# Kernel tuning notes

Hardware: AMD Instinct MI355X
Metric: run time of the kernel (lower is better)

The kernel has to match this reference:

```python
import jax, jax.numpy as jnp
import numpy as np

N_ATOMS = 8000
N_PAIRS = 80000
NF_IN = 32
NF_OUT = 32
N_DIST = 16
N_COMP = 4      # l_max=1: [l=0 (1), l=1 (3)] tensor components
N_INV = 2       # _invariant_counts[(2, 1)]
MIND_SOFT = 0.85
MAXD_SOFT = 5.0
HARD_CUTOFF = 6.5
GN_EPS = 1e-5


def _sensitivity(dist, mu, sigma):
    # HIP-NN style inverse-distance Gaussians with smooth cos^2 cutoff.
    inv_d = 1.0 / dist                                   # (P,)
    base = jnp.exp(-0.5 * ((inv_d[:, None] - mu) / sigma) ** 2)  # (P, n_dist)
    cut = jnp.where(dist < HARD_CUTOFF,
                    jnp.cos(0.5 * jnp.pi * dist / HARD_CUTOFF) ** 2, 0.0)
    return base * cut[:, None]


def setup_inputs() -> dict:
    key = jax.random.key(0)
    ks = jax.random.split(key, 10)
    in_features = jax.random.normal(ks[0], (N_ATOMS, NF_IN), jnp.float32)
    pair_first = jnp.sort(jax.random.randint(ks[1], (N_PAIRS,), 0, N_ATOMS))
    pair_second = jax.random.randint(ks[2], (N_PAIRS,), 0, N_ATOMS)
    dist_pairs = (0.5 + (HARD_CUTOFF - 0.5)
                  * jax.random.uniform(ks[3], (N_PAIRS,), jnp.float32))
    tensor_rhats = jax.random.normal(ks[4], (N_PAIRS, N_COMP), jnp.float32)
    # learned params
    sens_mu = jnp.linspace(1.0 / MAXD_SOFT, 1.0 / MIND_SOFT, N_DIST).astype(jnp.float32)
    sens_sigma = jnp.full((N_DIST,), float(sens_mu[1] - sens_mu[0]), jnp.float32)
    s_int = (2.0 / (N_DIST * NF_IN + NF_OUT)) ** 0.5
    int_weights = s_int * jax.random.normal(ks[5], (N_DIST, NF_OUT, NF_IN), jnp.float32)
    s_self = (2.0 / (NF_IN + NF_OUT)) ** 0.5
    selfint_w = s_self * jax.random.normal(ks[6], (NF_OUT, NF_IN), jnp.float32)
    selfint_b = jnp.zeros((NF_OUT,), jnp.float32)
    s_mix = (2.0 / (N_INV * NF_OUT + NF_OUT)) ** 0.5
    mixing_weights = s_mix * jax.random.normal(ks[7], (NF_OUT, N_INV, NF_OUT), jnp.float32)
    gn_weight = jnp.ones((N_INV * NF_OUT,), jnp.float32)
    gn_bias = jnp.zeros((N_INV * NF_OUT,), jnp.float32)
    return {
        "in_features": in_features, "tensor_rhats": tensor_rhats,
        "dist_pairs": dist_pairs, "int_weights": int_weights,
        "selfint_w": selfint_w, "selfint_b": selfint_b,
        "mixing_weights": mixing_weights, "gn_weight": gn_weight,
        "gn_bias": gn_bias, "sens_mu": sens_mu, "sens_sigma": sens_sigma,
        "pair_first": pair_first, "pair_second": pair_second,
    }


def reference(in_features, tensor_rhats, dist_pairs, int_weights,
              selfint_w, selfint_b, mixing_weights, gn_weight, gn_bias,
              sens_mu, sens_sigma, pair_first, pair_second):
    n_atoms = in_features.shape[0]
    # self interaction (Linear)
    self_part = in_features @ selfint_w.T + selfint_b          # (N, nf_out)
    # tensor sensitivities: (P, n_comp, n_dist) -> flat (P, n_comp*n_dist)
    sense = _sensitivity(dist_pairs, sens_mu, sens_sigma)      # (P, n_dist)
    sense_flat = (tensor_rhats[:, :, None] * sense[:, None, :]).reshape(
        -1, N_COMP * N_DIST)
    # envsum: env[a, s, f] = sum_{p: pair_first[p]=a} sense_flat[p, s] * feat[pair_second[p], f]
    feat_j = in_features[pair_second]                          # (P, nf_in)
    contrib = sense_flat[:, :, None] * feat_j[:, None, :]      # (P, S, nf_in)
    env = jax.ops.segment_sum(contrib, pair_first, num_segments=n_atoms)
    # interaction weights contraction
    w_rs = jnp.transpose(int_weights, (0, 2, 1)).reshape(N_DIST * NF_IN, NF_OUT)
    env_rs = env.reshape(n_atoms * N_COMP, N_DIST * NF_IN)
    tf = (env_rs @ w_rs).reshape(n_atoms, N_COMP, NF_OUT)
    tf = jnp.transpose(tf, (0, 2, 1))                          # (N, nf_out, n_comp)
    # HopInvariantLayer (n_max=2, l_max=1): [l=0 scalar, |l=1 vector|^2]
    invariants = jnp.stack(
        [tf[..., 0], jnp.sum(tf[..., 1:] ** 2, axis=-1)], axis=-1)  # (N, nf_out, 2)
    # GroupNorm over channels (n_inv groups of nf_out channels)
    x = jnp.transpose(invariants, (0, 2, 1))                   # (N, n_inv, nf_out)
    mean = jnp.mean(x, axis=-1, keepdims=True)
    var = jnp.var(x, axis=-1, keepdims=True)
    xn = (x - mean) / jnp.sqrt(var + GN_EPS)
    xn = xn * gn_weight.reshape(N_INV, NF_OUT) + gn_bias.reshape(N_INV, NF_OUT)
    norm_inv = jnp.transpose(xn, (0, 2, 1)).reshape(n_atoms, NF_OUT * N_INV)
    mix = norm_inv @ mixing_weights.reshape(NF_OUT * N_INV, NF_OUT)
    return mix + self_part
```

## Files before the change

### kernel.cpp

```cpp
#include <hip/hip_runtime.h>
#include <hip/hip_bf16.h>
#include <stdint.h>

#define GN_EPS 1e-5f

typedef __fp16 half2_t __attribute__((ext_vector_type(2)));
typedef __fp16 v8h __attribute__((ext_vector_type(8)));
typedef float v4f __attribute__((ext_vector_type(4)));
union U32H2 { uint32_t u; half2_t h; };
union U4V8 { uint4 u; v8h h; };
union UF { uint32_t u; float f; };

__device__ __forceinline__ float ldin(const void* p, int i, bool bf) {
    if (bf) {
        UF c; c.u = ((uint32_t)((const uint16_t*)p)[i]) << 16;
        return c.f;
    }
    return ((const float*)p)[i];
}

__device__ __forceinline__ uint16_t f2bf(float x) {
    union { float f; uint32_t u; } c; c.f = x;
    uint32_t u = c.u;
    return (uint16_t)((u + 0x7FFFu + ((u >> 16) & 1u)) >> 16);
}

__device__ __forceinline__ bool detect_bf16(const void* gnw) {
    uint32_t det = *(const uint32_t*)gnw;
    return (det >> 16) == (det & 0xFFFFu);
}

__device__ __forceinline__ uint32_t pkh2(float lo, float hi) {
    U32H2 u; u.h = __builtin_amdgcn_cvt_pkrtz(lo, hi); return u.u;
}

__global__ __launch_bounds__(256) void k0_prep(
    const void* __restrict__ feat, const void* __restrict__ rhats,
    const void* __restrict__ dists, const void* __restrict__ intw,
    const void* __restrict__ selfw, const void* __restrict__ selfb,
    const void* __restrict__ mw, const void* __restrict__ gnw,
    const void* __restrict__ gnb, const void* __restrict__ mu,
    const void* __restrict__ sig, const int* __restrict__ pf,
    int* __restrict__ seg, uint32_t* __restrict__ Wmf,
    float* __restrict__ featf, float4* __restrict__ rc4,
    float2* __restrict__ dj2, const int* __restrict__ ps,
    float* __restrict__ mwf, uint32_t* __restrict__ selfh,
    float* __restrict__ gnwf, float* __restrict__ gnbf,
    float* __restrict__ selfbf, float* __restrict__ muf,
    float* __restrict__ isgf, int n_atoms, int n_pairs)
{
    const bool bf = detect_bf16(gnw);
    const int tid = blockIdx.x * 256 + threadIdx.x;

    if (tid < n_pairs) {
        int a0 = pf[tid];
        if (tid == 0) { for (int a = 0; a <= a0; ++a) seg[a] = 0; }
        if (tid + 1 < n_pairs) {
            int a1 = pf[tid + 1];
            for (int a = a0 + 1; a <= a1; ++a) seg[a] = tid + 1;
        } else {
            for (int a = a0 + 1; a <= n_atoms; ++a) seg[a] = n_pairs;
        }
        float dist = ldin(dists, tid, bf);
        float cd = __cosf(0.2416609733530613f * dist);
        float cut = (dist < 6.5f) ? cd * cd : 0.0f;
        float4 rc;
        rc.x = ldin(rhats, 4 * tid + 0, bf) * cut;
        rc.y = ldin(rhats, 4 * tid + 1, bf) * cut;
        rc.z = ldin(rhats, 4 * tid + 2, bf) * cut;
        rc.w = ldin(rhats, 4 * tid + 3, bf) * cut;
        rc4[tid] = rc;
        float2 dj; dj.x = 1.0f / dist; dj.y = __int_as_float(ps[tid]);
        dj2[tid] = dj;
    }
    {
        int i0 = tid * 4;
#pragma unroll
        for (int k = 0; k < 4; ++k) {
            int i = i0 + k;
            if (i < n_atoms * 32) featf[i] = ldin(feat, i, bf);
        }
    }
    if (tid < 8192) {
        int fp = tid & 15, d = (tid >> 4) & 15, o = tid >> 8;
        float wlo = ldin(intw, (d * 32 + o) * 32 + 2 * fp, bf);
        float whi = ldin(intw, (d * 32 + o) * 32 + 2 * fp + 1, bf);
        Wmf[tid] = pkh2(wlo, whi);
    }
    if (tid < 2048) mwf[tid] = ldin(mw, tid, bf);
    if (tid < 512) {
        int fp = tid & 15, o = tid >> 4;
        selfh[tid] = pkh2(ldin(selfw, o * 32 + 2 * fp, bf),
                          ldin(selfw, o * 32 + 2 * fp + 1, bf));
    }
    if (tid < 64) { gnwf[tid] = ldin(gnw, tid, bf); gnbf[tid] = ldin(gnb, tid, bf); }
    if (tid < 32) selfbf[tid] = ldin(selfb, tid, bf);
    if (tid < 16) { muf[tid] = ldin(mu, tid, bf); isgf[tid] = 1.0f / ldin(sig, tid, bf); }
}

__global__ __launch_bounds__(256, 4) void k2_main(
    const int* __restrict__ seg, const uint32_t* __restrict__ Wmf,
    const float* __restrict__ featf, const float4* __restrict__ rc4,
    const float2* __restrict__ dj2, const float* __restrict__ mwf,
    const uint32_t* __restrict__ selfh, const float* __restrict__ gnwf,
    const float* __restrict__ gnbf, const float* __restrict__ selfbf,
    const float* __restrict__ muf, const float* __restrict__ isgf,
    const void* __restrict__ gnw, void* __restrict__ out, int n_atoms)
{
    __shared__ uint32_t envs[16 * 256];
    __shared__ float tfs[4 * 32 * 4];
    __shared__ float selfs[4][32];
    __shared__ float mwTs[32 * 68];
    __shared__ float xns[4][64];

    const int t = threadIdx.x, wv = t >> 6, lane = t & 63;
    const int a0 = blockIdx.x * 4;
    int a = a0 + wv;
    const bool astore = (a < n_atoms);
    if (!astore) a = n_atoms - 1;

    {
        int o = t & 31, kc = t >> 5;
#pragma unroll
        for (int i = 0; i < 8; ++i) {
            int k = kc * 8 + i;
            mwTs[o * 68 + k] = mwf[k * 32 + o];
        }
    }

    const int dD = lane >> 2, fq = lane & 3;
    const float mu_d = muf[dD], isg_d = isgf[dD];

    float env[4][8];
#pragma unroll
    for (int c = 0; c < 4; ++c)
#pragma unroll
        for (int fl = 0; fl < 8; ++fl) env[c][fl] = 0.0f;

    const int s = seg[a], e = seg[a + 1];

    for (int p = s; p < e; p += 4) {
        float2 dj[4]; float4 rc[4];
#pragma unroll
        for (int i = 0; i < 4; ++i) {
            int pi = (p + i < e) ? p + i : e - 1;
            dj[i] = dj2[pi];
            float4 r = rc4[pi];
            if (p + i >= e) r = make_float4(0.f, 0.f, 0.f, 0.f);
            rc[i] = r;
        }
        float4 fa[4], fb[4];
#pragma unroll
        for (int i = 0; i < 4; ++i) {
            const float4* fr = (const float4*)(featf +
                (size_t)__float_as_int(dj[i].y) * 32) + fq * 2;
            fa[i] = fr[0]; fb[i] = fr[1];
        }
#pragma unroll
        for (int i = 0; i < 4; ++i) {
            float x = (dj[i].x - mu_d) * isg_d;
            float sd = __expf(-0.5f * x * x);
            float t0 = sd * rc[i].x, t1 = sd * rc[i].y;
            float t2 = sd * rc[i].z, t3 = sd * rc[i].w;
            float fj[8] = {fa[i].x, fa[i].y, fa[i].z, fa[i].w,
                           fb[i].x, fb[i].y, fb[i].z, fb[i].w};
#pragma unroll
            for (int fl = 0; fl < 8; ++fl) {
                env[0][fl] = fmaf(t0, fj[fl], env[0][fl]);
                env[1][fl] = fmaf(t1, fj[fl], env[1][fl]);
                env[2][fl] = fmaf(t2, fj[fl], env[2][fl]);
                env[3][fl] = fmaf(t3, fj[fl], env[3][fl]);
            }
        }
    }

    {
        const int ci = dD * 4 + fq;
#pragma unroll
        for (int c = 0; c < 4; ++c) {
            int m = wv * 4 + c;
            uint4 w;
            w.x = pkh2(env[c][0], env[c][1]);
            w.y = pkh2(env[c][2], env[c][3]);
            w.z = pkh2(env[c][4], env[c][5]);
            w.w = pkh2(env[c][6], env[c][7]);
            *(uint4*)&envs[m * 256 + ((ci ^ m) << 2)] = w;
        }
    }
    __syncthreads();

    const int mrow = lane & 15, quad = lane >> 4;
    const int tile = wv >> 1;
    const int og = tile * 16 + mrow;
    if ((wv & 1) == 0) {
        v4f acc = {0.f, 0.f, 0.f, 0.f};
        const uint4* wb = (const uint4*)Wmf + (og * 64 + quad);
#pragma unroll
        for (int kk = 0; kk < 16; ++kk) {
            int cia = kk * 4 + quad;
            U4V8 Af, Bf;
            Af.u = *(const uint4*)&envs[mrow * 256 + ((cia ^ mrow) << 2)];
            Bf.u = wb[kk * 4];
            acc = __builtin_amdgcn_mfma_f32_16x16x32_f16(Af.h, Bf.h, acc, 0, 0, 0);
        }
        float4 st; st.x = acc[0]; st.y = acc[1]; st.z = acc[2]; st.w = acc[3];
        *(float4*)&tfs[(quad * 32 + og) * 4] = st;
    } else {
        int ar = a0 + (mrow < 4 ? mrow : 0);
        if (ar >= n_atoms) ar = n_atoms - 1;
        const float4* fp4 = (const float4*)(featf + (size_t)ar * 32 + quad * 8);
        float4 x = fp4[0], y = fp4[1];
        U4V8 Af, Bf;
        Af.u = make_uint4(pkh2(x.x, x.y), pkh2(x.z, x.w),
                          pkh2(y.x, y.y), pkh2(y.z, y.w));
        Bf.u = *(const uint4*)(selfh + og * 16 + quad * 4);
        v4f acc = {0.f, 0.f, 0.f, 0.f};
        acc = __builtin_amdgcn_mfma_f32_16x16x32_f16(Af.h, Bf.h, acc, 0, 0, 0);
        if (quad == 0) {
#pragma unroll
            for (int r = 0; r < 4; ++r)
                selfs[r][og] = acc[r];
        }
    }
    __syncthreads();

    const int o = lane & 31, half = lane >> 5;
    float4 tf = *(const float4*)&tfs[(wv * 32 + o) * 4];
    float inv0 = tf.x;
    float inv1 = tf.y * tf.y + tf.z * tf.z + tf.w * tf.w;

    float s0 = inv0, q0 = inv0 * inv0, s1 = inv1, q1 = inv1 * inv1;
#pragma unroll
    for (int m = 16; m >= 1; m >>= 1) {
        s0 += __shfl_xor(s0, m, 32);
        q0 += __shfl_xor(q0, m, 32);
        s1 += __shfl_xor(s1, m, 32);
        q1 += __shfl_xor(q1, m, 32);
    }
    float mean0 = s0 * (1.f / 32.f), mean1 = s1 * (1.f / 32.f);
    float var0 = q0 * (1.f / 32.f) - mean0 * mean0;
    float var1 = q1 * (1.f / 32.f) - mean1 * mean1;
    float xn0 = (inv0 - mean0) * rsqrtf(var0 + GN_EPS);
    float xn1 = (inv1 - mean1) * rsqrtf(var1 + GN_EPS);
    xn0 = xn0 * gnwf[o] + gnbf[o];
    xn1 = xn1 * gnwf[32 + o] + gnbf[32 + o];

    if (half == 0) *(float2*)&xns[wv][2 * o] = make_float2(xn0, xn1);

    float mix = 0.0f;
#pragma unroll
    for (int c = 0; c < 16; ++c) {
        float4 xk = *(const float4*)&xns[wv][c * 4];
        float4 w4 = *(const float4*)&mwTs[o * 68 + c * 4];
        mix = fmaf(xk.x, w4.x, mix);
        mix = fmaf(xk.y, w4.y, mix);
        mix = fmaf(xk.z, w4.z, mix);
        mix = fmaf(xk.w, w4.w, mix);
    }

    float res = mix + selfs[wv][o] + selfbf[o];
    if (half == 0 && astore) {
        if (detect_bf16(gnw)) ((uint16_t*)out)[a * 32 + o] = f2bf(res);
        else                  ((float*)out)[a * 32 + o]    = res;
    }
}

extern "C" void kernel_launch(void* const* d_in, const int* in_sizes, int n_in,
                              void* d_out, int out_size, void* d_ws, size_t ws_size,
                              hipStream_t stream) {
    const void* feat  = d_in[0];
    const void* rhats = d_in[1];
    const void* dists = d_in[2];
    const void* intw  = d_in[3];
    const void* selfw = d_in[4];
    const void* selfb = d_in[5];
    const void* mw    = d_in[6];
    const void* gnw   = d_in[7];
    const void* gnb   = d_in[8];
    const void* mu    = d_in[9];
    const void* sig   = d_in[10];
    const int* pf     = (const int*)d_in[11];
    const int* ps     = (const int*)d_in[12];

    const int n_pairs = in_sizes[11];
    const int n_atoms = in_sizes[0] / 32;

    char* ws = (char*)d_ws;
    int*      seg    = (int*)(ws + 0);
    uint32_t* Wmf    = (uint32_t*)(ws + 32768);
    float*    featf  = (float*)(ws + 65536);
    float4*   rc4    = (float4*)(ws + 1089536);
    float2*   dj2    = (float2*)(ws + 2369536);
    float*    mwf    = (float*)(ws + 3009536);
    uint32_t* selfh  = (uint32_t*)(ws + 3017728);
    float*    gnwf   = (float*)(ws + 3021824);
    float*    gnbf   = (float*)(ws + 3022080);
    float*    selfbf = (float*)(ws + 3022336);
    float*    muf    = (float*)(ws + 3022464);
    float*    isgf   = (float*)(ws + 3022528);

    int thr = n_pairs;
    int feat_thr = (n_atoms * 32 + 3) / 4;
    if (feat_thr > thr) thr = feat_thr;
    if (thr < 8192) thr = 8192;
    hipLaunchKernelGGL(k0_prep, dim3((thr + 255) / 256), dim3(256), 0, stream,
                       feat, rhats, dists, intw, selfw, selfb, mw, gnw, gnb,
                       mu, sig, pf, seg, Wmf, featf, rc4, dj2, ps, mwf,
                       selfh, gnwf, gnbf, selfbf, muf, isgf, n_atoms, n_pairs);
    hipLaunchKernelGGL(k2_main, dim3((n_atoms + 3) / 4), dim3(256), 0, stream,
                       seg, Wmf, featf, rc4, dj2, mwf, selfh, gnwf, gnbf,
                       selfbf, muf, isgf, gnw, d_out, n_atoms);
}
```

Measured before the change: 110.3 us.

## Process eight atoms per block with half-wave per atom and global transposed mixing weights

Main kernel now maps each atom to 32 lanes (half a wave) instead of a full wave, so a 256-thread block handles 8 atoms. Each lane accumulates 16 features across 4 components, and the MFMA stage computes 32 rows using all four waves. The mixing-weight transpose moves into the prep kernel and is read directly from global memory, removing the per-block LDS staging. This halves the block count and amortizes per-block overhead, but it doubles per-lane registers, which may reduce occupancy. It also makes two atoms with different pair counts share one wave, which adds divergence.

```diff
diff --git a/kernel.cpp b/kernel.cpp
--- a/kernel.cpp
+++ b/kernel.cpp
@@ -44,7 +44,7 @@
     int* __restrict__ seg, uint32_t* __restrict__ Wmf,
     float* __restrict__ featf, float4* __restrict__ rc4,
     float2* __restrict__ dj2, const int* __restrict__ ps,
-    float* __restrict__ mwf, uint32_t* __restrict__ selfh,
+    float* __restrict__ mwT, uint32_t* __restrict__ selfh,
     float* __restrict__ gnwf, float* __restrict__ gnbf,
     float* __restrict__ selfbf, float* __restrict__ muf,
     float* __restrict__ isgf, int n_atoms, int n_pairs)
@@ -87,7 +87,10 @@
         float whi = ldin(intw, (d * 32 + o) * 32 + 2 * fp + 1, bf);
         Wmf[tid] = pkh2(wlo, whi);
     }
-    if (tid < 2048) mwf[tid] = ldin(mw, tid, bf);
+    if (tid < 2048) {
+        int k = tid & 63, o = tid >> 6;
+        mwT[tid] = ldin(mw, k * 32 + o, bf);
+    }
     if (tid < 512) {
         int fp = tid & 15, o = tid >> 4;
         selfh[tid] = pkh2(ldin(selfw, o * 32 + 2 * fp, bf),
@@ -101,71 +104,63 @@
 __global__ __launch_bounds__(256, 4) void k2_main(
     const int* __restrict__ seg, const uint32_t* __restrict__ Wmf,
     const float* __restrict__ featf, const float4* __restrict__ rc4,
-    const float2* __restrict__ dj2, const float* __restrict__ mwf,
+    const float2* __restrict__ dj2, const float* __restrict__ mwT,
     const uint32_t* __restrict__ selfh, const float* __restrict__ gnwf,
     const float* __restrict__ gnbf, const float* __restrict__ selfbf,
     const float* __restrict__ muf, const float* __restrict__ isgf,
     const void* __restrict__ gnw, void* __restrict__ out, int n_atoms)
 {
-    __shared__ uint32_t envs[16 * 256];
-    __shared__ float tfs[4 * 32 * 4];
-    __shared__ float selfs[4][32];
-    __shared__ float mwTs[32 * 68];
-    __shared__ float xns[4][64];
+    __shared__ uint32_t envs[32 * 256];
+    __shared__ float tfs[8 * 32 * 4];
+    __shared__ float selfs[8][32];
+    __shared__ float xns[8][64];
 
     const int t = threadIdx.x, wv = t >> 6, lane = t & 63;
-    const int a0 = blockIdx.x * 4;
-    int a = a0 + wv;
+    const int half = lane >> 5, l5 = lane & 31;
+    const int a0 = blockIdx.x * 8;
+    const int la = wv * 2 + half;
+    int a = a0 + la;
     const bool astore = (a < n_atoms);
     if (!astore) a = n_atoms - 1;
 
-    {
-        int o = t & 31, kc = t >> 5;
-#pragma unroll
-        for (int i = 0; i < 8; ++i) {
-            int k = kc * 8 + i;
-            mwTs[o * 68 + k] = mwf[k * 32 + o];
-        }
-    }
-
-    const int dD = lane >> 2, fq = lane & 3;
+    const int dD = l5 >> 1, fh = l5 & 1;
     const float mu_d = muf[dD], isg_d = isgf[dD];
 
-    float env[4][8];
+    float env[4][16];
 #pragma unroll
     for (int c = 0; c < 4; ++c)
 #pragma unroll
-        for (int fl = 0; fl < 8; ++fl) env[c][fl] = 0.0f;
+        for (int fl = 0; fl < 16; ++fl) env[c][fl] = 0.0f;
 
     const int s = seg[a], e = seg[a + 1];
 
-    for (int p = s; p < e; p += 4) {
-        float2 dj[4]; float4 rc[4];
-#pragma unroll
-        for (int i = 0; i < 4; ++i) {
+    for (int p = s; p < e; p += 2) {
+        float2 dj[2]; float4 rc[2];
+#pragma unroll
+        for (int i = 0; i < 2; ++i) {
             int pi = (p + i < e) ? p + i : e - 1;
             dj[i] = dj2[pi];
             float4 r = rc4[pi];
             if (p + i >= e) r = make_float4(0.f, 0.f, 0.f, 0.f);
             rc[i] = r;
         }
-        float4 fa[4], fb[4];
-#pragma unroll
-        for (int i = 0; i < 4; ++i) {
+        float4 fv[2][4];
+#pragma unroll
+        for (int i = 0; i < 2; ++i) {
             const float4* fr = (const float4*)(featf +
-                (size_t)__float_as_int(dj[i].y) * 32) + fq * 2;
-            fa[i] = fr[0]; fb[i] = fr[1];
-        }
-#pragma unroll
-        for (int i = 0; i < 4; ++i) {
+                (size_t)__float_as_int(dj[i].y) * 32) + fh * 4;
+#pragma unroll
+            for (int q = 0; q < 4; ++q) fv[i][q] = fr[q];
+        }
+#pragma unroll
+        for (int i = 0; i < 2; ++i) {
             float x = (dj[i].x - mu_d) * isg_d;
             float sd = __expf(-0.5f * x * x);
             float t0 = sd * rc[i].x, t1 = sd * rc[i].y;
             float t2 = sd * rc[i].z, t3 = sd * rc[i].w;
-            float fj[8] = {fa[i].x, fa[i].y, fa[i].z, fa[i].w,
-                           fb[i].x, fb[i].y, fb[i].z, fb[i].w};
-#pragma unroll
-            for (int fl = 0; fl < 8; ++fl) {
+            const float* fj = (const float*)fv[i];
+#pragma unroll
+            for (int fl = 0; fl < 16; ++fl) {
                 env[0][fl] = fmaf(t0, fj[fl], env[0][fl]);
                 env[1][fl] = fmaf(t1, fj[fl], env[1][fl]);
                 env[2][fl] = fmaf(t2, fj[fl], env[2][fl]);
@@ -175,38 +170,47 @@
     }
 
     {
-        const int ci = dD * 4 + fq;
+        const int ci0 = dD * 4 + fh * 2;
 #pragma unroll
         for (int c = 0; c < 4; ++c) {
-            int m = wv * 4 + c;
-            uint4 w;
-            w.x = pkh2(env[c][0], env[c][1]);
-            w.y = pkh2(env[c][2], env[c][3]);
-            w.z = pkh2(env[c][4], env[c][5]);
-            w.w = pkh2(env[c][6], env[c][7]);
-            *(uint4*)&envs[m * 256 + ((ci ^ m) << 2)] = w;
+            int m = la * 4 + c;
+            uint4 w0, w1;
+            w0.x = pkh2(env[c][0],  env[c][1]);
+            w0.y = pkh2(env[c][2],  env[c][3]);
+            w0.z = pkh2(env[c][4],  env[c][5]);
+            w0.w = pkh2(env[c][6],  env[c][7]);
+            w1.x = pkh2(env[c][8],  env[c][9]);
+            w1.y = pkh2(env[c][10], env[c][11]);
+            w1.z = pkh2(env[c][12], env[c][13]);
+            w1.w = pkh2(env[c][14], env[c][15]);
+            *(uint4*)&envs[m * 256 + (((ci0 + 0) ^ m) << 2)] = w0;
+            *(uint4*)&envs[m * 256 + (((ci0 + 1) ^ m) << 2)] = w1;
         }
     }
     __syncthreads();
 
     const int mrow = lane & 15, quad = lane >> 4;
-    const int tile = wv >> 1;
-    const int og = tile * 16 + mrow;
-    if ((wv & 1) == 0) {
+    {
+        const int rowg = (wv >> 1) * 16, tile = wv & 1;
+        const int og = tile * 16 + mrow;
+        const int grow = rowg + mrow;
         v4f acc = {0.f, 0.f, 0.f, 0.f};
         const uint4* wb = (const uint4*)Wmf + (og * 64 + quad);
 #pragma unroll
         for (int kk = 0; kk < 16; ++kk) {
             int cia = kk * 4 + quad;
             U4V8 Af, Bf;
-            Af.u = *(const uint4*)&envs[mrow * 256 + ((cia ^ mrow) << 2)];
+            Af.u = *(const uint4*)&envs[grow * 256 + ((cia ^ grow) << 2)];
             Bf.u = wb[kk * 4];
             acc = __builtin_amdgcn_mfma_f32_16x16x32_f16(Af.h, Bf.h, acc, 0, 0, 0);
         }
+        int atomD = (rowg >> 2) + quad;
         float4 st; st.x = acc[0]; st.y = acc[1]; st.z = acc[2]; st.w = acc[3];
-        *(float4*)&tfs[(quad * 32 + og) * 4] = st;
-    } else {
-        int ar = a0 + (mrow < 4 ? mrow : 0);
+        *(float4*)&tfs[(atomD * 32 + og) * 4] = st;
+    }
+    if (wv < 2) {
+        const int og = wv * 16 + mrow;
+        int ar = a0 + (mrow & 7);
         if (ar >= n_atoms) ar = n_atoms - 1;
         const float4* fp4 = (const float4*)(featf + (size_t)ar * 32 + quad * 8);
         float4 x = fp4[0], y = fp4[1];
@@ -216,16 +220,16 @@
         Bf.u = *(const uint4*)(selfh + og * 16 + quad * 4);
         v4f acc = {0.f, 0.f, 0.f, 0.f};
         acc = __builtin_amdgcn_mfma_f32_16x16x32_f16(Af.h, Bf.h, acc, 0, 0, 0);
-        if (quad == 0) {
-#pragma unroll
-            for (int r = 0; r < 4; ++r)
-                selfs[r][og] = acc[r];
+#pragma unroll
+        for (int reg = 0; reg < 4; ++reg) {
+            int r = quad * 4 + reg;
+            if (r < 8) selfs[r][og] = acc[reg];
         }
     }
     __syncthreads();
 
-    const int o = lane & 31, half = lane >> 5;
-    float4 tf = *(const float4*)&tfs[(wv * 32 + o) * 4];
+    const int o = l5;
+    float4 tf = *(const float4*)&tfs[(la * 32 + o) * 4];
     float inv0 = tf.x;
     float inv1 = tf.y * tf.y + tf.z * tf.z + tf.w * tf.w;
 
@@ -245,21 +249,22 @@
     xn0 = xn0 * gnwf[o] + gnbf[o];
     xn1 = xn1 * gnwf[32 + o] + gnbf[32 + o];
 
-    if (half == 0) *(float2*)&xns[wv][2 * o] = make_float2(xn0, xn1);
+    *(float2*)&xns[la][2 * o] = make_float2(xn0, xn1);
 
     float mix = 0.0f;
+    const float4* mrow4 = (const float4*)(mwT + o * 64);
 #pragma unroll
     for (int c = 0; c < 16; ++c) {
-        float4 xk = *(const float4*)&xns[wv][c * 4];
-        float4 w4 = *(const float4*)&mwTs[o * 68 + c * 4];
+        float4 xk = *(const float4*)&xns[la][c * 4];
+        float4 w4 = mrow4[c];
         mix = fmaf(xk.x, w4.x, mix);
         mix = fmaf(xk.y, w4.y, mix);
         mix = fmaf(xk.z, w4.z, mix);
         mix = fmaf(xk.w, w4.w, mix);
     }
 
-    float res = mix + selfs[wv][o] + selfbf[o];
-    if (half == 0 && astore) {
+    float res = mix + selfs[la][o] + selfbf[o];
+    if (astore) {
         if (detect_bf16(gnw)) ((uint16_t*)out)[a * 32 + o] = f2bf(res);
         else                  ((float*)out)[a * 32 + o]    = res;
     }
@@ -291,7 +296,7 @@
     float*    featf  = (float*)(ws + 65536);
     float4*   rc4    = (float4*)(ws + 1089536);
     float2*   dj2    = (float2*)(ws + 2369536);
-    float*    mwf    = (float*)(ws + 3009536);
+    float*    mwT    = (float*)(ws + 3009536);
     uint32_t* selfh  = (uint32_t*)(ws + 3017728);
     float*    gnwf   = (float*)(ws + 3021824);
     float*    gnbf   = (float*)(ws + 3022080);
@@ -305,9 +310,9 @@
     if (thr < 8192) thr = 8192;
     hipLaunchKernelGGL(k0_prep, dim3((thr + 255) / 256), dim3(256), 0, stream,
                        feat, rhats, dists, intw, selfw, selfb, mw, gnw, gnb,
-                       mu, sig, pf, seg, Wmf, featf, rc4, dj2, ps, mwf,
+                       mu, sig, pf, seg, Wmf, featf, rc4, dj2, ps, mwT,
                        selfh, gnwf, gnbf, selfbf, muf, isgf, n_atoms, n_pairs);
-    hipLaunchKernelGGL(k2_main, dim3((n_atoms + 3) / 4), dim3(256), 0, stream,
-                       seg, Wmf, featf, rc4, dj2, mwf, selfh, gnwf, gnbf,
+    hipLaunchKernelGGL(k2_main, dim3((n_atoms + 7) / 8), dim3(256), 0, stream,
+                       seg, Wmf, featf, rc4, dj2, mwT, selfh, gnwf, gnbf,
                        selfbf, muf, isgf, gnw, d_out, n_atoms);
 }
```

New measurement: 113.4 us. 2.8% more time.
